# Performance work log

Hardware: AMD Instinct MI355X
Metric: run time of the kernel (lower is better)

Reference implementation:

```python
import jax, jax.numpy as jnp
import numpy as np
from jax import lax

TAU = 0.05
N_ITERS = 4
TOPL = 64


def l2norm(x, axis):
    return x / (jnp.linalg.norm(x, axis=axis, keepdims=True) + 1e-6)


def setup_inputs() -> dict:
    key = jax.random.key(0)
    ks = jax.random.split(key, 8)
    B, N, Ck, Cv, H, W, L = 2, 4, 64, 512, 64, 64, 256
    qk = jax.random.normal(ks[0], (B, Ck, H, W), jnp.float32)
    qv = jax.random.normal(ks[1], (B, Cv, H, W), jnp.float32)
    qv_mem = jax.random.normal(ks[2], (B, N, Cv, H, W), jnp.float32)
    masks = jax.random.uniform(ks[3], (B, N, 2, H, W), jnp.float32)
    # random_init: normal(0, sqrt(2/L)) then l2norm over Ck (dim=-2)
    kappa0 = jax.random.normal(ks[4], (B, N, 2, Ck, L), jnp.float32) * np.sqrt(2.0 / L).astype(np.float32)
    kappa0 = l2norm(kappa0, axis=-2)
    nu0 = jnp.zeros((B, N, 2, Cv, L), jnp.float32)
    zita0 = jnp.full((B, N, 2, 1, L), 1e-6, jnp.float32)
    Cin = 2 * Cv + 2 * TOPL  # 1152
    Wf = jax.random.normal(ks[5], (Cv, Cin, 3, 3), jnp.float32) * 0.02
    bf = jnp.zeros((Cv,), jnp.float32)
    Wa = jax.random.normal(ks[6], (Cv, Cin, 3, 3), jnp.float32) * 0.02
    ba = jnp.zeros((Cv,), jnp.float32)
    return {"qk": qk, "qv": qv, "qv_mem": qv_mem, "masks": masks,
            "kappa0": kappa0, "nu0": nu0, "zita0": zita0,
            "Wf": Wf, "bf": bf, "Wa": Wa, "ba": ba}


def reference(qk, qv, qv_mem, masks, kappa0, nu0, zita0, Wf, bf, Wa, ba):
    B, Ck, H, W = qk.shape
    N = masks.shape[1]
    Cv = qv.shape[1]
    L = kappa0.shape[-1]
    HW = H * W

    # ---- swem: EM iterations (torch runs these under no_grad) ----
    x = qk.reshape(B, 1, 1, Ck, HW)            # (B,1,1,Ck,HW)
    m = masks.reshape(B, N, 2, HW, 1)          # (B,N,2,HW,1)
    x_t = jnp.swapaxes(x, -2, -1)              # (B,1,1,HW,Ck)
    x_t_n = l2norm(x_t, axis=-1)

    weights = m
    kappa = kappa0
    z = None
    zita = None
    for i in range(N_ITERS):
        # swe_step: softmax((z - max)/tau) == softmax(z/tau), stable
        kn = l2norm(kappa, axis=-2)
        zz = jnp.matmul(x_t, kn)               # (B,N,2,HW,L)
        zz = jax.nn.softmax(zz / TAU, axis=-1) * weights
        # swm_step
        zita = zita0 + zz.sum(axis=-2, keepdims=True)            # (B,N,2,1,L)
        kappa = (zita0 * kappa0 + jnp.matmul(x, zz)) / zita      # (B,N,2,Ck,L)
        z = zz
        if i < N_ITERS - 1:
            # sww_step
            kn = l2norm(kappa, axis=-2)
            s = jnp.matmul(x_t_n, kn)                            # (B,N,2,HW,L)
            mx = jnp.max(s, axis=-1, keepdims=True)
            mx = jnp.max(mx, axis=2, keepdims=True)
            s_exp = jnp.exp((s - mx) / TAU)
            sum_exp = s_exp.sum(axis=-1, keepdims=True)          # (B,N,2,HW,1)
            props = sum_exp / sum_exp.sum(axis=2, keepdims=True)
            weights = m * (1.0 - props)

    mv_flat = qv_mem.reshape(B, N, 1, Cv, HW)                    # (B,N,1,Cv,HW)
    nu = (zita0 * nu0 + jnp.matmul(mv_flat, z)) / zita           # (B,N,2,Cv,L)

    # ---- matching / get_affinity ----
    qk_n = l2norm(qk, axis=1)
    mk = l2norm(kappa, axis=-2)
    qk_ = qk_n.reshape(B, 1, 1, Ck, HW)
    aff = jnp.matmul(jnp.swapaxes(mk, -2, -1), qk_)              # (B,N,2,L,HW)
    mx = jnp.max(aff, axis=2, keepdims=True)
    mx = jnp.max(mx, axis=3, keepdims=True)
    exp_aff = jnp.exp((aff - mx) / TAU)
    p_aff = exp_aff / exp_aff.sum(axis=(2, 3), keepdims=True)
    p_aff = p_aff.reshape(B, N, 2 * L, HW)

    # ---- perm_inv_feat: top-l over L, cumulative sums (vectorized) ----
    ea = exp_aff.reshape(B * N, 2, L, H, W)
    sorted_aff = lax.top_k(jnp.moveaxis(ea, 2, -1), TOPL)[0]     # (BN,2,H,W,TOPL) desc
    feat = jnp.cumsum(sorted_aff, axis=-1)
    Sf = feat[:, 0] / (feat[:, 0] + feat[:, 1])                  # (BN,H,W,TOPL)
    Sf = jnp.moveaxis(Sf, -1, 1)                                 # (BN,TOPL,H,W)
    S = jnp.concatenate([Sf, 1.0 - Sf], axis=1)                  # (BN,2*TOPL,H,W)

    # ---- memory readout ----
    mv2 = jnp.swapaxes(nu, 2, 3).reshape(B, N, Cv, 2 * L)
    mem_out = jnp.matmul(mv2, p_aff).reshape(B * N, Cv, H, W)

    qv_e = jnp.broadcast_to(qv[:, None], (B, N, Cv, H, W)).reshape(B * N, Cv, H, W)
    fin = jnp.concatenate([mem_out, qv_e, S], axis=1)            # (BN, 2*Cv+2*TOPL, H, W)

    # ---- FeatureFusionLayer: gated 3x3 convs ----
    dn = ('NCHW', 'OIHW', 'NCHW')
    f = lax.conv_general_dilated(fin, Wf, (1, 1), 'SAME', dimension_numbers=dn) + bf[None, :, None, None]
    a = lax.conv_general_dilated(fin, Wa, (1, 1), 'SAME', dimension_numbers=dn) + ba[None, :, None, None]
    return f * jax.nn.sigmoid(a)
```

## Files before the change

kernel.cpp:

```cpp
#include <hip/hip_runtime.h>
#include <hip/hip_bf16.h>
#include <math.h>


typedef __attribute__((ext_vector_type(8))) short bf16x8;
typedef __attribute__((ext_vector_type(4))) float f32x4;
typedef __attribute__((ext_vector_type(16))) float f32x16;

static __device__ __forceinline__ short f2b(float f){
  __hip_bfloat16 h = __float2bfloat16(f);
  short s; __builtin_memcpy(&s, &h, 2); return s;
}
static __device__ __forceinline__ unsigned pack2(float lo, float hi){
  return (unsigned)(unsigned short)f2b(lo) | ((unsigned)(unsigned short)f2b(hi) << 16);
}

static __device__ __forceinline__ float wred_max(float v){
  #pragma unroll
  for (int off = 32; off > 0; off >>= 1) v = fmaxf(v, __shfl_xor(v, off));
  return v;
}
static __device__ __forceinline__ float wred_sum(float v){
  #pragma unroll
  for (int off = 32; off > 0; off >>= 1) v += __shfl_xor(v, off);
  return v;
}

static __device__ __forceinline__ void gload_lds16(const short* g, short* l){
  __builtin_amdgcn_global_load_lds((const __attribute__((address_space(1))) unsigned int*)(g),
                                   (__attribute__((address_space(3))) unsigned int*)(l),
                                   16, 0, 0);
}

#define FMA16(X0,X1,X2,X3,KV) \
  acc[0]+=X0.x*KV; acc[1]+=X0.y*KV; acc[2]+=X0.z*KV; acc[3]+=X0.w*KV; \
  acc[4]+=X1.x*KV; acc[5]+=X1.y*KV; acc[6]+=X1.z*KV; acc[7]+=X1.w*KV; \
  acc[8]+=X2.x*KV; acc[9]+=X2.y*KV; acc[10]+=X2.z*KV; acc[11]+=X2.w*KV; \
  acc[12]+=X3.x*KV; acc[13]+=X3.y*KV; acc[14]+=X3.z*KV; acc[15]+=X3.w*KV;


__global__ void k_prep_x(const float* __restrict__ qk, float* __restrict__ xT, float* __restrict__ xTn){
  int idx = blockIdx.x*256 + threadIdx.x;
  int b = idx >> 12, hw = idx & 4095;
  float v[64]; float ss = 0.f;
  #pragma unroll
  for (int k=0;k<64;k++){ v[k] = qk[((size_t)b*64 + k)*4096 + hw]; ss += v[k]*v[k]; }
  float inv = 1.f/(sqrtf(ss) + 1e-6f);
  #pragma unroll
  for (int k=0;k<64;k++){ xT[(size_t)idx*64 + k] = v[k]; xTn[(size_t)idx*64 + k] = v[k]*inv; }
}

__global__ void k_init_w_kn(const float* __restrict__ masks, const float* __restrict__ kappa0,
                            float* __restrict__ wts, float* __restrict__ kn){
  int t = blockIdx.x*256 + threadIdx.x;
  if (t < 16*4096) wts[t] = masks[t];
  if (t < 16*256){
    int bng = t >> 8, l = t & 255;
    float ss = 0.f;
    #pragma unroll 4
    for (int k=0;k<64;k++){ float v = kappa0[((size_t)bng*64 + k)*256 + l]; ss += v*v; }
    float inv = 1.f/(sqrtf(ss) + 1e-6f);
    #pragma unroll 4
    for (int k=0;k<64;k++) kn[((size_t)bng*64 + k)*256 + l] = kappa0[((size_t)bng*64 + k)*256 + l]*inv;
  }
}

__global__ void k_prep_wt2(const float* __restrict__ Wsrc, short* __restrict__ Wt2, int conv){
  int t = blockIdx.x*256 + threadIdx.x;
  int j = t & 7;
  int cvl = (t >> 3) & 63;
  int kh = (t >> 9) & 1;
  int rest = t >> 10;
  int r = rest % 9;
  int tile = rest / 9;
  int cb = tile % 72;
  int cvb = tile / 72;
  int cv = cvb*64 + cvl;
  int cin = cb*16 + kh*8 + j;
  Wt2[((size_t)tile*2 + conv)*9216 + (r*2 + kh)*512 + cvl*8 + j] = f2b(Wsrc[((size_t)cv*1152 + cin)*9 + r]);
}

__global__ void k_qv_fin(const float* __restrict__ qv, unsigned* __restrict__ fin32){
  int t = blockIdx.x*256 + threadIdx.x;
  int bn = t >> 20;
  int rem = t & 1048575;
  int p = rem >> 12;
  int hw = rem & 4095;
  int b = bn >> 2;
  float lo = qv[((size_t)b*512 + 2*p)*4096 + hw];
  float hi = qv[((size_t)b*512 + 2*p + 1)*4096 + hw];
  fin32[(size_t)bn*2359296 + (size_t)(256 + p)*4096 + hw] = pack2(lo, hi);
}


__global__ __launch_bounds__(256) void k_zz(const float* __restrict__ xT, const float* __restrict__ kn,
                                            const float* __restrict__ wts, float* __restrict__ zzb){
  int blk = blockIdx.x;
  int bng = blk >> 8;
  int hw0 = (blk & 255) * 16;
  int b = bng >> 3;
  int t = threadIdx.x;
  int lane = t & 63, wid = t >> 6;
  __shared__ float xs[64][16];
  __shared__ float redm[4], reds[4];
  {
    int k = t & 63, pq = t >> 6;
    #pragma unroll
    for (int p = pq; p < 16; p += 4)
      xs[k][p] = xT[((size_t)b*4096 + hw0 + p)*64 + k];
  }
  float acc[16];
  #pragma unroll
  for (int p=0;p<16;p++) acc[p] = 0.f;
  __syncthreads();
  const float* knp = kn + (size_t)bng*16384 + t;
  #pragma unroll 2
  for (int k=0;k<64;k++){
    float knv = knp[k*256];
    float4 x0 = *(const float4*)&xs[k][0];
    float4 x1 = *(const float4*)&xs[k][4];
    float4 x2 = *(const float4*)&xs[k][8];
    float4 x3 = *(const float4*)&xs[k][12];
    FMA16(x0,x1,x2,x3,knv)
  }
  #pragma unroll
  for (int p=0;p<16;p++){
    float v = acc[p];
    float m = wred_max(v);
    if (lane==0) redm[wid] = m;
    __syncthreads();
    m = fmaxf(fmaxf(redm[0],redm[1]), fmaxf(redm[2],redm[3]));
    float e = __expf((v - m) * 20.0f);
    float s = wred_sum(e);
    if (lane==0) reds[wid] = s;
    __syncthreads();
    s = reds[0]+reds[1]+reds[2]+reds[3];
    float wgt = wts[bng*4096 + hw0 + p];
    zzb[((size_t)bng*4096 + hw0 + p)*256 + t] = e/s*wgt;
  }
}

__global__ __launch_bounds__(1024) void k_part(const float* __restrict__ qk, const float* __restrict__ zzb,
                                               float* __restrict__ kpart, float* __restrict__ zpart){
  int bng = blockIdx.x >> 4, ch = blockIdx.x & 15;
  int b = bng >> 3;
  int t = threadIdx.x; int l = t & 255; int kq = t >> 8;
  __shared__ float xs[64][80];
  float acc[16];
  #pragma unroll
  for (int j=0;j<16;j++) acc[j]=0.f;
  float zs = 0.f;
  for (int sc=0; sc<4; sc++){
    int hwb = ch*256 + sc*64;
    __syncthreads();
    {
      int hw_l = t & 63, kk = t >> 6;
      #pragma unroll
      for (int k = kk; k < 64; k += 16)
        xs[hw_l][k] = qk[((size_t)b*64 + k)*4096 + hwb + hw_l];
    }
    __syncthreads();
    #pragma unroll 2
    for (int hw_l=0; hw_l<64; hw_l++){
      float zv = zzb[((size_t)bng*4096 + hwb + hw_l)*256 + l];
      zs += zv;
      const float* xp = &xs[hw_l][kq*16];
      float4 x0 = *(const float4*)(xp);
      float4 x1 = *(const float4*)(xp+4);
      float4 x2 = *(const float4*)(xp+8);
      float4 x3 = *(const float4*)(xp+12);
      FMA16(x0,x1,x2,x3,zv)
    }
  }
  #pragma unroll
  for (int j=0;j<16;j++)
    kpart[(((size_t)bng*16 + ch)*64 + kq*16 + j)*256 + l] = acc[j];
  if (kq == 0) zpart[((size_t)bng*16 + ch)*256 + l] = zs;
}

__global__ __launch_bounds__(1024) void k_fin(const float* __restrict__ kpart, const float* __restrict__ zpart,
                                              const float* __restrict__ kappa0, const float* __restrict__ zita0,
                                              float* __restrict__ kn, float* __restrict__ zita){
  int bng = blockIdx.x; int t = threadIdx.x; int l = t & 255; int kq = t >> 8;
  float z0 = zita0[bng*256 + l];
  float zs = z0;
  #pragma unroll
  for (int ch=0; ch<16; ch++) zs += zpart[((size_t)bng*16 + ch)*256 + l];
  if (kq==0) zita[bng*256 + l] = zs;
  float inv = 1.f/zs;
  float kap[16]; float ss = 0.f;
  #pragma unroll
  for (int j=0;j<16;j++){
    int k = kq*16 + j;
    float a = z0 * kappa0[((size_t)bng*64 + k)*256 + l];
    #pragma unroll
    for (int ch=0; ch<16; ch++) a += kpart[(((size_t)bng*16 + ch)*64 + k)*256 + l];
    float kv = a*inv; kap[j] = kv; ss += kv*kv;
  }
  __shared__ float ssr[4][256];
  ssr[kq][l] = ss;
  __syncthreads();
  float tot = ssr[0][l]+ssr[1][l]+ssr[2][l]+ssr[3][l];
  float ninv = 1.f/(sqrtf(tot) + 1e-6f);
  #pragma unroll
  for (int j=0;j<16;j++) kn[((size_t)bng*64 + kq*16 + j)*256 + l] = kap[j]*ninv;
}

__global__ __launch_bounds__(512) void k_sww(const float* __restrict__ xTn, const float* __restrict__ kn,
                                             const float* __restrict__ masks, float* __restrict__ wts){
  int blk = blockIdx.x;
  int bnI = blk >> 8;
  int hw0 = (blk & 255)*16;
  int b = bnI >> 2;
  int t = threadIdx.x;
  int lane = t & 63, wid = t >> 6;
  int g = t >> 8; int l = t & 255;
  int bng = bnI*2 + g;
  __shared__ float xs[64][16];
  __shared__ float redm[8], reds[8];
  {
    int k = t & 63, pq = t >> 6;
    #pragma unroll
    for (int p = pq; p < 16; p += 8)
      xs[k][p] = xTn[((size_t)b*4096 + hw0 + p)*64 + k];
  }
  float knr[64];
  const float* knp = kn + (size_t)bng*16384 + l;
  #pragma unroll
  for (int k=0;k<64;k++) knr[k] = knp[k*256];
  float acc[16];
  #pragma unroll
  for (int p=0;p<16;p++) acc[p]=0.f;
  __syncthreads();
  #pragma unroll 2
  for (int k=0;k<64;k++){
    float knv = knr[k];
    float4 x0 = *(const float4*)&xs[k][0];
    float4 x1 = *(const float4*)&xs[k][4];
    float4 x2 = *(const float4*)&xs[k][8];
    float4 x3 = *(const float4*)&xs[k][12];
    FMA16(x0,x1,x2,x3,knv)
  }
  #pragma unroll
  for (int p=0;p<16;p++){
    float v = acc[p];
    float m = wred_max(v);
    if (lane==0) redm[wid] = m;
    __syncthreads();
    m = fmaxf(fmaxf(fmaxf(redm[0],redm[1]),fmaxf(redm[2],redm[3])),
              fmaxf(fmaxf(redm[4],redm[5]),fmaxf(redm[6],redm[7])));
    float e = __expf((v - m) * 20.0f);
    float s = wred_sum(e);
    if (lane==0) reds[wid] = s;
    __syncthreads();
    float s0 = reds[0]+reds[1]+reds[2]+reds[3];
    float s1 = reds[4]+reds[5]+reds[6]+reds[7];
    if (lane==0 && (wid==0 || wid==4)){
      float sg = g ? s1 : s0;
      wts[bng*4096 + hw0 + p] = masks[bng*4096 + hw0 + p]*(1.f - sg/(s0+s1));
    }
  }
}

__global__ __launch_bounds__(512) void k_aff(const float* __restrict__ xTn, const float* __restrict__ kn,
                                             float* __restrict__ paff){
  int blk = blockIdx.x;
  int bnI = blk >> 8;
  int hw0 = (blk & 255)*16;
  int b = bnI >> 2;
  int t = threadIdx.x;
  int lane = t & 63, wid = t >> 6;
  int g = t >> 8; int l = t & 255;
  int bng = bnI*2 + g;
  __shared__ float xs[64][16];
  __shared__ float redm[8], reds[8];
  {
    int k = t & 63, pq = t >> 6;
    #pragma unroll
    for (int p = pq; p < 16; p += 8)
      xs[k][p] = xTn[((size_t)b*4096 + hw0 + p)*64 + k];
  }
  float knr[64];
  const float* knp = kn + (size_t)bng*16384 + l;
  #pragma unroll
  for (int k=0;k<64;k++) knr[k] = knp[k*256];
  float acc[16];
  #pragma unroll
  for (int p=0;p<16;p++) acc[p]=0.f;
  __syncthreads();
  #pragma unroll 2
  for (int k=0;k<64;k++){
    float knv = knr[k];
    float4 x0 = *(const float4*)&xs[k][0];
    float4 x1 = *(const float4*)&xs[k][4];
    float4 x2 = *(const float4*)&xs[k][8];
    float4 x3 = *(const float4*)&xs[k][12];
    FMA16(x0,x1,x2,x3,knv)
  }
  #pragma unroll
  for (int p=0;p<16;p++){
    float v = acc[p];
    float m = wred_max(v);
    if (lane==0) redm[wid] = m;
    __syncthreads();
    m = fmaxf(fmaxf(fmaxf(redm[0],redm[1]),fmaxf(redm[2],redm[3])),
              fmaxf(fmaxf(redm[4],redm[5]),fmaxf(redm[6],redm[7])));
    float e = __expf((v - m) * 20.0f);
    float s = wred_sum(e);
    if (lane==0) reds[wid] = s;
    __syncthreads();
    float tot = reds[0]+reds[1]+reds[2]+reds[3]+reds[4]+reds[5]+reds[6]+reds[7];
    paff[((size_t)bnI*4096 + hw0 + p)*512 + t] = e/tot;
  }
}


static __device__ __forceinline__ float topk_cum(float va, float vb, float vc, float vd, int lane){
  float run = 0.f, cme = 0.f;
  #pragma unroll 2
  for (int tt=0; tt<64; tt++){
    float m = fmaxf(fmaxf(va,vb), fmaxf(vc,vd));
    float wm = wred_max(m);
    run += wm;
    if (lane == tt) cme = run;
    unsigned long long ball = __ballot(m == wm);
    int wl = __ffsll(ball) - 1;
    if (lane == wl){
      if (va == wm) va = -1.f;
      else if (vb == wm) vb = -1.f;
      else if (vc == wm) vc = -1.f;
      else vd = -1.f;
    }
  }
  return cme;
}

__global__ __launch_bounds__(256) void k_topk(const float* __restrict__ paff, unsigned* __restrict__ fin32){
  int wid = threadIdx.x >> 6, lane = threadIdx.x & 63;
  int px = blockIdx.x*4 + wid;
  int bn = px >> 12, hw = px & 4095;
  const float* row = paff + (size_t)px*512;
  float4 a0 = *(const float4*)(row + lane*4);
  float4 a1 = *(const float4*)(row + 256 + lane*4);
  float c0 = topk_cum(a0.x,a0.y,a0.z,a0.w, lane);
  float c1 = topk_cum(a1.x,a1.y,a1.z,a1.w, lane);
  float sf = c0/(c0+c1);
  float sf2 = __shfl_down(sf, 1);
  if (!(lane & 1)){
    size_t base = (size_t)bn*2359296;
    fin32[base + (size_t)(512 + (lane>>1))*4096 + hw] = pack2(sf, sf2);
    fin32[base + (size_t)(544 + (lane>>1))*4096 + hw] = pack2(1.f - sf, 1.f - sf2);
  }
}


__global__ __launch_bounds__(256) void k_nu(const float* __restrict__ qvm, const float* __restrict__ zzb,
                                            const float* __restrict__ nu0, const float* __restrict__ zita0,
                                            const float* __restrict__ zita, short* __restrict__ mv2){
  constexpr int AP = 40;
  __shared__ short lA[64*AP];
  __shared__ short lB[64*AP];
  int blk = blockIdx.x;
  int bng = blk >> 5, cvb = (blk >> 2) & 7, lb = blk & 3;
  int bn = bng >> 1, g = bng & 1;
  int t = threadIdx.x, lane = t & 63, w = t >> 6;
  int wm = w >> 1, wn = w & 1;
  int quad = lane >> 4, fr = lane & 15;
  f32x4 acc[2][2] = {};
  const float* Ab = qvm + ((size_t)bn*512 + cvb*64)*4096;
  const float* Bb = zzb + (size_t)bng*4096*256 + lb*64;
  int arow = t >> 2, acg = (t & 3)*8;
  int bhw = t & 31, blg = (t >> 5)*8;
  for (int k0 = 0; k0 < 4096; k0 += 32){
    __syncthreads();
    {
      const float* s = Ab + (size_t)arow*4096 + k0 + acg;
      float4 f0 = *(const float4*)s, f1 = *(const float4*)(s+4);
      bf16x8 v;
      v[0]=f2b(f0.x); v[1]=f2b(f0.y); v[2]=f2b(f0.z); v[3]=f2b(f0.w);
      v[4]=f2b(f1.x); v[5]=f2b(f1.y); v[6]=f2b(f1.z); v[7]=f2b(f1.w);
      *(bf16x8*)&lA[arow*AP + acg] = v;
    }
    {
      const float* s = Bb + (size_t)(k0 + bhw)*256 + blg;
      float4 f0 = *(const float4*)s, f1 = *(const float4*)(s+4);
      lB[(blg+0)*AP + bhw] = f2b(f0.x);
      lB[(blg+1)*AP + bhw] = f2b(f0.y);
      lB[(blg+2)*AP + bhw] = f2b(f0.z);
      lB[(blg+3)*AP + bhw] = f2b(f0.w);
      lB[(blg+4)*AP + bhw] = f2b(f1.x);
      lB[(blg+5)*AP + bhw] = f2b(f1.y);
      lB[(blg+6)*AP + bhw] = f2b(f1.z);
      lB[(blg+7)*AP + bhw] = f2b(f1.w);
    }
    __syncthreads();
    int koff = quad*8;
    bf16x8 a0 = *(const bf16x8*)&lA[(wm*32 +  0 + fr)*AP + koff];
    bf16x8 a1 = *(const bf16x8*)&lA[(wm*32 + 16 + fr)*AP + koff];
    bf16x8 b0 = *(const bf16x8*)&lB[(wn*32 +  0 + fr)*AP + koff];
    bf16x8 b1 = *(const bf16x8*)&lB[(wn*32 + 16 + fr)*AP + koff];
    acc[0][0] = __builtin_amdgcn_mfma_f32_16x16x32_bf16(a0,b0,acc[0][0],0,0,0);
    acc[0][1] = __builtin_amdgcn_mfma_f32_16x16x32_bf16(a0,b1,acc[0][1],0,0,0);
    acc[1][0] = __builtin_amdgcn_mfma_f32_16x16x32_bf16(a1,b0,acc[1][0],0,0,0);
    acc[1][1] = __builtin_amdgcn_mfma_f32_16x16x32_bf16(a1,b1,acc[1][1],0,0,0);
  }
  #pragma unroll
  for (int mf=0; mf<2; mf++)
  #pragma unroll
  for (int nf=0; nf<2; nf++)
  #pragma unroll
  for (int r=0;r<4;r++){
    int cv = cvb*64 + wm*32 + mf*16 + quad*4 + r;
    int l  = lb*64 + wn*32 + nf*16 + fr;
    float c = acc[mf][nf][r];
    float z0 = zita0[bng*256 + l];
    float nv = (z0 * nu0[((size_t)bng*512 + cv)*256 + l] + c) / zita[bng*256 + l];
    mv2[((size_t)bn*512 + cv)*512 + g*256 + l] = f2b(nv);
  }
}

__global__ __launch_bounds__(256) void k_mem(const short* __restrict__ mv2, const float* __restrict__ paff,
                                             unsigned* __restrict__ fin32){
  constexpr int BP = 40;
  __shared__ short lB[256*BP];
  int blk = blockIdx.x;
  int bn = blk >> 7, cvb = (blk >> 4) & 7, hwb = blk & 15;
  int t = threadIdx.x, lane = t & 63, w = t >> 6;
  int quad = lane >> 4, fr = lane & 15;
  f32x4 acc[4][4] = {};
  const short* Ab = mv2 + ((size_t)bn*512 + cvb*64)*512;
  const float* Bb = paff + ((size_t)bn*4096 + hwb*256)*512;
  for (int k0=0; k0<512; k0+=32){
    __syncthreads();
    {
      const float* s = Bb + (size_t)t*512 + k0;
      #pragma unroll
      for (int q=0;q<4;q++){
        float4 f0 = *(const float4*)(s + q*8);
        float4 f1 = *(const float4*)(s + q*8 + 4);
        bf16x8 v;
        v[0]=f2b(f0.x); v[1]=f2b(f0.y); v[2]=f2b(f0.z); v[3]=f2b(f0.w);
        v[4]=f2b(f1.x); v[5]=f2b(f1.y); v[6]=f2b(f1.z); v[7]=f2b(f1.w);
        *(bf16x8*)&lB[t*BP + q*8] = v;
      }
    }
    __syncthreads();
    int koff = quad*8;
    bf16x8 af[4];
    #pragma unroll
    for (int mf=0; mf<4; mf++)
      af[mf] = *(const bf16x8*)(Ab + (size_t)(mf*16 + fr)*512 + k0 + koff);
    #pragma unroll
    for (int nf=0; nf<4; nf++){
      bf16x8 bv = *(const bf16x8*)&lB[(w*64 + nf*16 + fr)*BP + koff];
      #pragma unroll
      for (int mf=0; mf<4; mf++)
        acc[mf][nf] = __builtin_amdgcn_mfma_f32_16x16x32_bf16(af[mf], bv, acc[mf][nf],0,0,0);
    }
  }
  #pragma unroll
  for (int mf=0;mf<4;mf++)
  #pragma unroll
  for (int nf=0;nf<4;nf++){
    int hw = hwb*256 + w*64 + nf*16 + fr;
    int p0 = cvb*32 + mf*8 + quad*2;
    unsigned lo = pack2(acc[mf][nf][0], acc[mf][nf][1]);
    unsigned hi = pack2(acc[mf][nf][2], acc[mf][nf][3]);
    fin32[(size_t)bn*2359296 + (size_t)p0*4096 + hw] = lo;
    fin32[(size_t)bn*2359296 + (size_t)(p0+1)*4096 + hw] = hi;
  }
}


#define CONV_STAGE_DECL \
  unsigned stg[3][4];
#define CONV_LOAD_STG(CB) { \
    _Pragma("unroll") \
    for (int i = 0; i < 3; i++){ \
      int tk = wv*3 + i; \
      int skh = (tk >= 6) ? 1 : 0; \
      int srow = tk - skh*6; \
      int gy = y0 - 1 + srow; \
      bool ok = (gy >= 0 && gy < 64); \
      _Pragma("unroll") \
      for (int pj = 0; pj < 4; pj++) \
        stg[i][pj] = ok ? finB[(size_t)((CB)*8 + skh*4 + pj)*4096 + gy*64 + lane] : 0u; \
    } }
#define CONV_WRITE_STG { \
    _Pragma("unroll") \
    for (int i = 0; i < 3; i++){ \
      int tk = wv*3 + i; \
      int skh = (tk >= 6) ? 1 : 0; \
      int srow = tk - skh*6; \
      uint4 v; v.x = stg[i][0]; v.y = stg[i][1]; v.z = stg[i][2]; v.w = stg[i][3]; \
      *(uint4*)&lFu[((skh*6 + srow)*66 + lane + 1)*4] = v; \
    } }
#define CONV_DMA_W(CB) { \
    const short* src = Wslice + (size_t)(CB)*18432 + lane*8; \
    _Pragma("unroll") \
    for (int i = 0; i < 9; i++){ \
      int idx = wv*9 + i; \
      gload_lds16(src + idx*512, &wbuf[idx*512]); \
    } }
#define CONV_COMPUTE { \
    __builtin_amdgcn_s_setprio(1); \
    _Pragma("unroll 3") \
    for (int r9 = 0; r9 < 9; r9++){ \
      int dy = r9/3, dx = r9 - dy*3; \
      bf16x8 f0 = *(const bf16x8*)(wbuf + r9*1024 + kh*512 + ln*8); \
      bf16x8 f1 = *(const bf16x8*)(wbuf + r9*1024 + kh*512 + ln*8 + 256); \
      bf16x8 a0 = *(const bf16x8*)(wbuf + 9216 + r9*1024 + kh*512 + ln*8); \
      bf16x8 a1 = *(const bf16x8*)(wbuf + 9216 + r9*1024 + kh*512 + ln*8 + 256); \
      int row = wv + dy; \
      _Pragma("unroll") \
      for (int xh = 0; xh < 2; xh++){ \
        bf16x8 bv = *(const bf16x8*)((const short*)lFu + (((kh*6 + row)*66 + xh*32 + ln + dx)*8)); \
        accF[0][xh] = __builtin_amdgcn_mfma_f32_32x32x16_bf16(f0, bv, accF[0][xh],0,0,0); \
        accF[1][xh] = __builtin_amdgcn_mfma_f32_32x32x16_bf16(f1, bv, accF[1][xh],0,0,0); \
        accA[0][xh] = __builtin_amdgcn_mfma_f32_32x32x16_bf16(a0, bv, accA[0][xh],0,0,0); \
        accA[1][xh] = __builtin_amdgcn_mfma_f32_32x32x16_bf16(a1, bv, accA[1][xh],0,0,0); \
      } \
    } \
    __builtin_amdgcn_s_setprio(0); }
#define CONV_HALO_ZERO \
  if (t < 96){ \
    int pj = t & 3; int side = (t >> 2) & 1; int row = (t >> 3) % 6; int khz = t / 48; \
    lFu[((khz*6 + row)*66 + (side ? 65 : 0))*4 + pj] = 0u; \
  }

__global__ __launch_bounds__(256, 2) void k_convu(const unsigned* __restrict__ fin32,
                                                  const short* __restrict__ Wt2,
                                                  float* __restrict__ U){
  __shared__ __attribute__((aligned(16))) unsigned lFu[2*6*66*4];
  __shared__ __attribute__((aligned(16))) short wbuf[2*9216];
  int blk = blockIdx.x;
  int h = blk >> 8, b = (blk >> 7) & 1, cvb = (blk >> 4) & 7, yb = blk & 15;
  int t = threadIdx.x, lane = t & 63, wv = t >> 6;
  int ln = lane & 31, kh = lane >> 5;
  int y0 = yb*4;
  f32x16 accF[2][2] = {}, accA[2][2] = {};
  const unsigned* finB = fin32 + (size_t)(b*4)*2359296;
  const short* Wslice = Wt2 + (size_t)cvb*72*18432;
  CONV_HALO_ZERO
  CONV_STAGE_DECL
  for (int i = 0; i < 16; i++){
    int cb = 32 + h*16 + i;
    CONV_LOAD_STG(cb)
    __syncthreads();
    CONV_WRITE_STG
    CONV_DMA_W(cb)
    __syncthreads();
    CONV_COMPUTE
  }
  int y = y0 + wv;
  #pragma unroll
  for (int mf = 0; mf < 2; mf++)
  #pragma unroll
  for (int xh = 0; xh < 2; xh++){
    int x = xh*32 + ln;
    #pragma unroll
    for (int reg = 0; reg < 16; reg++){
      int cv = cvb*64 + mf*32 + 4*kh + 8*(reg>>2) + (reg&3);
      size_t o = (size_t)cv*4096 + (size_t)y*64 + x;
      U[((size_t)(h*2 + 0)*2 + b)*2097152 + o] = accF[mf][xh][reg];
      U[((size_t)(h*2 + 1)*2 + b)*2097152 + o] = accA[mf][xh][reg];
    }
  }
}

__global__ __launch_bounds__(256, 2) void k_conv(const unsigned* __restrict__ fin32,
                                                 const short* __restrict__ Wt2,
                                                 const float* __restrict__ bfv, const float* __restrict__ bav,
                                                 const float* __restrict__ U,
                                                 float* __restrict__ out){
  __shared__ __attribute__((aligned(16))) unsigned lFu[2*6*66*4];
  __shared__ __attribute__((aligned(16))) short wbuf[2*9216];
  int blk = blockIdx.x;
  int bn = blk >> 7, cvb = (blk >> 4) & 7, yb = blk & 15;
  int t = threadIdx.x, lane = t & 63, wv = t >> 6;
  int ln = lane & 31, kh = lane >> 5;
  int y0 = yb*4;
  f32x16 accF[2][2] = {}, accA[2][2] = {};
  const unsigned* finB = fin32 + (size_t)bn*2359296;
  const short* Wslice = Wt2 + (size_t)cvb*72*18432;
  CONV_HALO_ZERO
  CONV_STAGE_DECL
  for (int i = 0; i < 40; i++){
    int cb = (i < 32) ? i : i + 32;
    CONV_LOAD_STG(cb)
    __syncthreads();
    CONV_WRITE_STG
    CONV_DMA_W(cb)
    __syncthreads();
    CONV_COMPUTE
  }
  int y = y0 + wv;
  int b = bn >> 2;
  #pragma unroll
  for (int mf = 0; mf < 2; mf++)
  #pragma unroll
  for (int xh = 0; xh < 2; xh++){
    int x = xh*32 + ln;
    #pragma unroll
    for (int reg = 0; reg < 16; reg++){
      int cv = cvb*64 + mf*32 + 4*kh + 8*(reg>>2) + (reg&3);
      size_t o = (size_t)cv*4096 + (size_t)y*64 + x;
      float fv = accF[mf][xh][reg] + bfv[cv]
               + U[((size_t)0*2 + b)*2097152 + o] + U[((size_t)2*2 + b)*2097152 + o];
      float av = accA[mf][xh][reg] + bav[cv]
               + U[((size_t)1*2 + b)*2097152 + o] + U[((size_t)3*2 + b)*2097152 + o];
      out[((size_t)bn*512 + cv)*4096 + (size_t)y*64 + x] = fv/(1.f + __expf(-av));
    }
  }
}


extern "C" void kernel_launch(void* const* d_in, const int* in_sizes, int n_in,
                              void* d_out, int out_size, void* d_ws, size_t ws_size,
                              hipStream_t stream){
  const float* qk     = (const float*)d_in[0];
  const float* qv     = (const float*)d_in[1];
  const float* qvm    = (const float*)d_in[2];
  const float* masks  = (const float*)d_in[3];
  const float* kappa0 = (const float*)d_in[4];
  const float* nu0    = (const float*)d_in[5];
  const float* zita0  = (const float*)d_in[6];
  const float* Wf     = (const float*)d_in[7];
  const float* bfb    = (const float*)d_in[8];
  const float* Wa     = (const float*)d_in[9];
  const float* bab    = (const float*)d_in[10];
  float* out = (float*)d_out;

  float* ws    = (float*)d_ws;
  float* zzb   = ws;
  float* kpart = zzb + 16777216;
  float* zpart = kpart + 4194304;
  float* kn    = zpart + 65536;
  float* zita  = kn + 262144;
  float* wts   = zita + 4096;
  float* xT    = wts + 65536;
  float* xTn   = xT + 524288;
  short* mv2   = (short*)(xTn + 524288);
  unsigned* fin32 = (unsigned*)(mv2 + 4194304);
  short* Wt2   = (short*)(fin32 + 18874368);
  float* U     = zzb;

  k_prep_x<<<32, 256, 0, stream>>>(qk, xT, xTn);
  k_init_w_kn<<<256, 256, 0, stream>>>(masks, kappa0, wts, kn);
  k_prep_wt2<<<20736, 256, 0, stream>>>(Wf, Wt2, 0);
  k_prep_wt2<<<20736, 256, 0, stream>>>(Wa, Wt2, 1);
  k_qv_fin<<<32768, 256, 0, stream>>>(qv, fin32);

  for (int it = 0; it < 4; ++it){
    k_zz<<<4096, 256, 0, stream>>>(xT, kn, wts, zzb);
    k_part<<<256, 1024, 0, stream>>>(qk, zzb, kpart, zpart);
    k_fin<<<16, 1024, 0, stream>>>(kpart, zpart, kappa0, zita0, kn, zita);
    if (it < 3) k_sww<<<2048, 512, 0, stream>>>(xTn, kn, masks, wts);
  }

  k_nu<<<512, 256, 0, stream>>>(qvm, zzb, nu0, zita0, zita, mv2);
  k_aff<<<2048, 512, 0, stream>>>(xTn, kn, zzb );
  k_topk<<<8192, 256, 0, stream>>>(zzb, fin32);
  k_mem<<<1024, 256, 0, stream>>>(mv2, zzb, fin32);
  k_convu<<<512, 256, 0, stream>>>(fin32, Wt2, U);
  k_conv<<<1024, 256, 0, stream>>>(fin32, Wt2, bfb, bab, U, out);
}
```

Before: 2.220 ms.

## Coalesce weight prep via LDS, stage zz in LDS, widen k_nu N-tile

The two weight-transpose launches become a single kernel that reads each conv weight tile with coalesced float4 loads into shared memory and writes bf16x8 vectors, replacing scattered strided reads. k_part now stages zz rows in shared memory in chunks of 16 before the FMA loop, which adds syncs but no longer reads global memory per FMA step. k_nu doubles its L tile to 128 per block, halving the grid and reusing the A fragments across four MFMA columns. These are three unrelated changes aimed at memory traffic and reuse, at the cost of more LDS per block and lower occupancy.

```diff
diff --git a/kernel.cpp b/kernel.cpp
--- a/kernel.cpp
+++ b/kernel.cpp
@@ -65,19 +65,42 @@
   }
 }
 
-__global__ void k_prep_wt2(const float* __restrict__ Wsrc, short* __restrict__ Wt2, int conv){
-  int t = blockIdx.x*256 + threadIdx.x;
-  int j = t & 7;
-  int cvl = (t >> 3) & 63;
-  int kh = (t >> 9) & 1;
-  int rest = t >> 10;
-  int r = rest % 9;
-  int tile = rest / 9;
+__global__ __launch_bounds__(256) void k_prep_wt2b(const float* __restrict__ Wf, const float* __restrict__ Wa,
+                                                   short* __restrict__ Wt2){
+  __shared__ float wsl[64][145];
+  int blk = blockIdx.x;
+  int conv = blk & 1;
+  int tile = blk >> 1;
   int cb = tile % 72;
   int cvb = tile / 72;
-  int cv = cvb*64 + cvl;
-  int cin = cb*16 + kh*8 + j;
-  Wt2[((size_t)tile*2 + conv)*9216 + (r*2 + kh)*512 + cvl*8 + j] = f2b(Wsrc[((size_t)cv*1152 + cin)*9 + r]);
+  const float* Wsrc = conv ? Wa : Wf;
+  int t = threadIdx.x;
+  int cvl = t >> 2, part = t & 3;
+  const float* src = Wsrc + ((size_t)(cvb*64 + cvl)*1152 + cb*16)*9;
+  #pragma unroll
+  for (int i = 0; i < 9; i++){
+    float4 v = *(const float4*)(src + part*4 + i*16);
+    wsl[cvl][part*4 + i*16 + 0] = v.x;
+    wsl[cvl][part*4 + i*16 + 1] = v.y;
+    wsl[cvl][part*4 + i*16 + 2] = v.z;
+    wsl[cvl][part*4 + i*16 + 3] = v.w;
+  }
+  __syncthreads();
+  short* obase = Wt2 + ((size_t)tile*2 + conv)*9216;
+  #pragma unroll
+  for (int i = 0; i < 5; i++){
+    int item = t + i*256;
+    if (item < 1152){
+      int rk = item >> 6;
+      int r = rk >> 1, kh = rk & 1;
+      int c2 = item & 63;
+      bf16x8 v;
+      #pragma unroll
+      for (int j = 0; j < 8; j++)
+        v[j] = f2b(wsl[c2][(kh*8 + j)*9 + r]);
+      *(bf16x8*)(obase + (size_t)item*8) = v;
+    }
+  }
 }
 
 __global__ void k_qv_fin(const float* __restrict__ qv, unsigned* __restrict__ fin32){
@@ -146,6 +169,7 @@
   int b = bng >> 3;
   int t = threadIdx.x; int l = t & 255; int kq = t >> 8;
   __shared__ float xs[64][80];
+  __shared__ float zlds[16][256];
   float acc[16];
   #pragma unroll
   for (int j=0;j<16;j++) acc[j]=0.f;
@@ -159,17 +183,27 @@
       for (int k = kk; k < 64; k += 16)
         xs[hw_l][k] = qk[((size_t)b*64 + k)*4096 + hwb + hw_l];
     }
-    __syncthreads();
-    #pragma unroll 2
-    for (int hw_l=0; hw_l<64; hw_l++){
-      float zv = zzb[((size_t)bng*4096 + hwb + hw_l)*256 + l];
-      zs += zv;
-      const float* xp = &xs[hw_l][kq*16];
-      float4 x0 = *(const float4*)(xp);
-      float4 x1 = *(const float4*)(xp+4);
-      float4 x2 = *(const float4*)(xp+8);
-      float4 x3 = *(const float4*)(xp+12);
-      FMA16(x0,x1,x2,x3,zv)
+    for (int chunk=0; chunk<4; chunk++){
+      #pragma unroll
+      for (int i=0;i<4;i++){
+        int e = t + i*1024;
+        int hh = e >> 8, l2 = e & 255;
+        zlds[hh][l2] = zzb[((size_t)bng*4096 + hwb + chunk*16 + hh)*256 + l2];
+      }
+      __syncthreads();
+      #pragma unroll 2
+      for (int hh=0; hh<16; hh++){
+        int hw_l = chunk*16 + hh;
+        float zv = zlds[hh][l];
+        zs += zv;
+        const float* xp = &xs[hw_l][kq*16];
+        float4 x0 = *(const float4*)(xp);
+        float4 x1 = *(const float4*)(xp+4);
+        float4 x2 = *(const float4*)(xp+8);
+        float4 x3 = *(const float4*)(xp+12);
+        FMA16(x0,x1,x2,x3,zv)
+      }
+      __syncthreads();
     }
   }
   #pragma unroll
@@ -359,16 +393,16 @@
                                             const float* __restrict__ zita, short* __restrict__ mv2){
   constexpr int AP = 40;
   __shared__ short lA[64*AP];
-  __shared__ short lB[64*AP];
+  __shared__ short lB[128*AP];
   int blk = blockIdx.x;
-  int bng = blk >> 5, cvb = (blk >> 2) & 7, lb = blk & 3;
+  int bng = blk >> 4, cvb = (blk >> 1) & 7, lb = blk & 1;
   int bn = bng >> 1, g = bng & 1;
   int t = threadIdx.x, lane = t & 63, w = t >> 6;
   int wm = w >> 1, wn = w & 1;
   int quad = lane >> 4, fr = lane & 15;
-  f32x4 acc[2][2] = {};
+  f32x4 acc[2][4] = {};
   const float* Ab = qvm + ((size_t)bn*512 + cvb*64)*4096;
-  const float* Bb = zzb + (size_t)bng*4096*256 + lb*64;
+  const float* Bb = zzb + (size_t)bng*4096*256 + lb*128;
   int arow = t >> 2, acg = (t & 3)*8;
   int bhw = t & 31, blg = (t >> 5)*8;
   for (int k0 = 0; k0 < 4096; k0 += 32){
@@ -381,37 +415,39 @@
       v[4]=f2b(f1.x); v[5]=f2b(f1.y); v[6]=f2b(f1.z); v[7]=f2b(f1.w);
       *(bf16x8*)&lA[arow*AP + acg] = v;
     }
-    {
-      const float* s = Bb + (size_t)(k0 + bhw)*256 + blg;
+    #pragma unroll
+    for (int h = 0; h < 2; h++){
+      int l0 = h*64 + blg;
+      const float* s = Bb + (size_t)(k0 + bhw)*256 + l0;
       float4 f0 = *(const float4*)s, f1 = *(const float4*)(s+4);
-      lB[(blg+0)*AP + bhw] = f2b(f0.x);
-      lB[(blg+1)*AP + bhw] = f2b(f0.y);
-      lB[(blg+2)*AP + bhw] = f2b(f0.z);
-      lB[(blg+3)*AP + bhw] = f2b(f0.w);
-      lB[(blg+4)*AP + bhw] = f2b(f1.x);
-      lB[(blg+5)*AP + bhw] = f2b(f1.y);
-      lB[(blg+6)*AP + bhw] = f2b(f1.z);
-      lB[(blg+7)*AP + bhw] = f2b(f1.w);
+      lB[(l0+0)*AP + bhw] = f2b(f0.x);
+      lB[(l0+1)*AP + bhw] = f2b(f0.y);
+      lB[(l0+2)*AP + bhw] = f2b(f0.z);
+      lB[(l0+3)*AP + bhw] = f2b(f0.w);
+      lB[(l0+4)*AP + bhw] = f2b(f1.x);
+      lB[(l0+5)*AP + bhw] = f2b(f1.y);
+      lB[(l0+6)*AP + bhw] = f2b(f1.z);
+      lB[(l0+7)*AP + bhw] = f2b(f1.w);
     }
     __syncthreads();
     int koff = quad*8;
     bf16x8 a0 = *(const bf16x8*)&lA[(wm*32 +  0 + fr)*AP + koff];
     bf16x8 a1 = *(const bf16x8*)&lA[(wm*32 + 16 + fr)*AP + koff];
-    bf16x8 b0 = *(const bf16x8*)&lB[(wn*32 +  0 + fr)*AP + koff];
-    bf16x8 b1 = *(const bf16x8*)&lB[(wn*32 + 16 + fr)*AP + koff];
-    acc[0][0] = __builtin_amdgcn_mfma_f32_16x16x32_bf16(a0,b0,acc[0][0],0,0,0);
-    acc[0][1] = __builtin_amdgcn_mfma_f32_16x16x32_bf16(a0,b1,acc[0][1],0,0,0);
-    acc[1][0] = __builtin_amdgcn_mfma_f32_16x16x32_bf16(a1,b0,acc[1][0],0,0,0);
-    acc[1][1] = __builtin_amdgcn_mfma_f32_16x16x32_bf16(a1,b1,acc[1][1],0,0,0);
+    #pragma unroll
+    for (int nf=0; nf<4; nf++){
+      bf16x8 bv = *(const bf16x8*)&lB[(wn*64 + nf*16 + fr)*AP + koff];
+      acc[0][nf] = __builtin_amdgcn_mfma_f32_16x16x32_bf16(a0,bv,acc[0][nf],0,0,0);
+      acc[1][nf] = __builtin_amdgcn_mfma_f32_16x16x32_bf16(a1,bv,acc[1][nf],0,0,0);
+    }
   }
   #pragma unroll
   for (int mf=0; mf<2; mf++)
   #pragma unroll
-  for (int nf=0; nf<2; nf++)
+  for (int nf=0; nf<4; nf++)
   #pragma unroll
   for (int r=0;r<4;r++){
     int cv = cvb*64 + wm*32 + mf*16 + quad*4 + r;
-    int l  = lb*64 + wn*32 + nf*16 + fr;
+    int l  = lb*128 + wn*64 + nf*16 + fr;
     float c = acc[mf][nf][r];
     float z0 = zita0[bng*256 + l];
     float nv = (z0 * nu0[((size_t)bng*512 + cv)*256 + l] + c) / zita[bng*256 + l];
@@ -647,8 +683,7 @@
 
   k_prep_x<<<32, 256, 0, stream>>>(qk, xT, xTn);
   k_init_w_kn<<<256, 256, 0, stream>>>(masks, kappa0, wts, kn);
-  k_prep_wt2<<<20736, 256, 0, stream>>>(Wf, Wt2, 0);
-  k_prep_wt2<<<20736, 256, 0, stream>>>(Wa, Wt2, 1);
+  k_prep_wt2b<<<1152, 256, 0, stream>>>(Wf, Wa, Wt2);
   k_qv_fin<<<32768, 256, 0, stream>>>(qv, fin32);
 
   for (int it = 0; it < 4; ++it){
@@ -658,7 +693,7 @@
     if (it < 3) k_sww<<<2048, 512, 0, stream>>>(xTn, kn, masks, wts);
   }
 
-  k_nu<<<512, 256, 0, stream>>>(qvm, zzb, nu0, zita0, zita, mv2);
+  k_nu<<<256, 256, 0, stream>>>(qvm, zzb, nu0, zita0, zita, mv2);
   k_aff<<<2048, 512, 0, stream>>>(xTn, kn, zzb );
   k_topk<<<8192, 256, 0, stream>>>(zzb, fin32);
   k_mem<<<1024, 256, 0, stream>>>(mv2, zzb, fin32);
```

Result: no change. 2.223 ms (+0.2%).
